# Performance work log

Hardware: AMD Instinct MI355X
Metric: run time of the kernel (lower is better)

The kernel has to match this reference:

```python
import jax, jax.numpy as jnp
import numpy as np

D_MODEL = 256
N_HEAD = 4
HEAD_DIM = D_MODEL // N_HEAD  # 64


def setup_inputs() -> dict:
    key = jax.random.key(0)
    kx, kw, kb = jax.random.split(key, 3)
    x = jax.random.normal(kx, (4, 2048, D_MODEL), dtype=jnp.float32)
    # nn.Linear(256, 768): weight [768, 256], bias [768]
    bound = 1.0 / np.sqrt(D_MODEL)
    W_qkv = jax.random.uniform(kw, (3 * D_MODEL, D_MODEL), dtype=jnp.float32, minval=-bound, maxval=bound)
    b_qkv = jax.random.uniform(kb, (3 * D_MODEL,), dtype=jnp.float32, minval=-bound, maxval=bound)
    return {"x": x, "W_qkv": W_qkv, "b_qkv": b_qkv}


def reference(x, W_qkv, b_qkv):
    B, S, _ = x.shape
    # fused QKV projection: [B, S, 3*D]
    qkv = jnp.einsum("bsd,ed->bse", x, W_qkv) + b_qkv
    q, k, v = jnp.split(qkv, 3, axis=-1)
    # [B, S, D] -> [B, H, S, Dh]
    def to_heads(t):
        return t.reshape(B, S, N_HEAD, HEAD_DIM).transpose(0, 2, 1, 3)
    q, k, v = to_heads(q), to_heads(k), to_heads(v)
    scale = 1.0 / np.sqrt(HEAD_DIM)
    # scores [B, H, S, S]
    scores = jnp.einsum("bhqd,bhkd->bhqk", q, k) * scale
    attn = jax.nn.softmax(scores, axis=-1)
    out = jnp.einsum("bhqk,bhkd->bhqd", attn, v)  # [B, H, S, Dh]
    return out
```

## Files before the change

kernel.cpp:

```cpp
#include <hip/hip_runtime.h>

#define BB 4
#define SS 2048
#define DM 256
#define NH 4
#define DH 64
#define NROW (BB*SS)
#define NE   (3*DM)
#define BH   (BB*NH)
#define HEAD_ELEMS (BH*SS*DH)
#define NQROWS (BH*SS)
#define NKZ 4

typedef _Float16 half_t;
typedef __attribute__((ext_vector_type(8))) _Float16 half8;
typedef __attribute__((ext_vector_type(4))) _Float16 half4;
typedef __attribute__((ext_vector_type(4))) float floatx4;

#define KPAD 72

#define QK_SCALE 0.18033688011112042f
#define EXP2(x) __builtin_amdgcn_exp2f(x)
#define DEFER_THR 8.0f

__global__ __launch_bounds__(256) void prep(const float* __restrict__ x,
                                            const float* __restrict__ W,
                                            half_t* __restrict__ xh,
                                            half_t* __restrict__ xl,
                                            half_t* __restrict__ wh) {
    int gtid = blockIdx.x * 256 + threadIdx.x;
    {
        int i = gtid * 4;
        float4 v = *(const float4*)&x[i];
        half4 h, l;
        h.x = (half_t)v.x; l.x = (half_t)(v.x - (float)h.x);
        h.y = (half_t)v.y; l.y = (half_t)(v.y - (float)h.y);
        h.z = (half_t)v.z; l.z = (half_t)(v.z - (float)h.z);
        h.w = (half_t)v.w; l.w = (half_t)(v.w - (float)h.w);
        *(half4*)&xh[i] = h;
        *(half4*)&xl[i] = l;
    }
    if (gtid < NE * DM / 4) {
        int i = gtid * 4;
        float4 v = *(const float4*)&W[i];
        half4 h;
        h.x = (half_t)v.x; h.y = (half_t)v.y;
        h.z = (half_t)v.z; h.w = (half_t)v.w;
        *(half4*)&wh[i] = h;
    }
}

__global__ __launch_bounds__(256) void qkv_proj(const half_t* __restrict__ xh,
                                                const half_t* __restrict__ xl,
                                                const half_t* __restrict__ whg,
                                                const float* __restrict__ bias,
                                                half_t* __restrict__ qh,
                                                half_t* __restrict__ kh,
                                                half_t* __restrict__ vt) {
    __shared__ __align__(16) half_t Xh[64 * KPAD];
    __shared__ __align__(16) half_t Xl[64 * KPAD];
    __shared__ __align__(16) half_t Wh[64 * KPAD];

    const int rb   = blockIdx.x * 64;
    const int nb   = blockIdx.y * 64;
    const int tid  = threadIdx.x;
    const int wid  = tid >> 6;
    const int lane = tid & 63;
    const int quad = lane >> 4;
    const int col  = lane & 15;

    floatx4 acc[4];
    #pragma unroll
    for (int t = 0; t < 4; ++t) acc[t] = (floatx4){0.f, 0.f, 0.f, 0.f};

    for (int k0 = 0; k0 < DM; k0 += 64) {
        __syncthreads();
        #pragma unroll
        for (int i = 0; i < 2; ++i) {
            int gi = tid + 256 * i;
            int r  = gi >> 3;
            int c8 = (gi & 7) * 8;
            *(half8*)&Xh[r * KPAD + c8] = *(const half8*)&xh[(size_t)(rb + r) * DM + k0 + c8];
            *(half8*)&Xl[r * KPAD + c8] = *(const half8*)&xl[(size_t)(rb + r) * DM + k0 + c8];
            *(half8*)&Wh[r * KPAD + c8] = *(const half8*)&whg[(size_t)(nb + r) * DM + k0 + c8];
        }
        __syncthreads();

        half8 ah0 = *(const half8*)&Xh[(wid * 16 + col) * KPAD + quad * 8];
        half8 ah1 = *(const half8*)&Xh[(wid * 16 + col) * KPAD + 32 + quad * 8];
        half8 al0 = *(const half8*)&Xl[(wid * 16 + col) * KPAD + quad * 8];
        half8 al1 = *(const half8*)&Xl[(wid * 16 + col) * KPAD + 32 + quad * 8];

        #pragma unroll
        for (int t = 0; t < 4; ++t) {
            half8 bh0 = *(const half8*)&Wh[(t * 16 + col) * KPAD + quad * 8];
            half8 bh1 = *(const half8*)&Wh[(t * 16 + col) * KPAD + 32 + quad * 8];
            acc[t] = __builtin_amdgcn_mfma_f32_16x16x32_f16(ah0, bh0, acc[t], 0, 0, 0);
            acc[t] = __builtin_amdgcn_mfma_f32_16x16x32_f16(ah1, bh1, acc[t], 0, 0, 0);
            acc[t] = __builtin_amdgcn_mfma_f32_16x16x32_f16(al0, bh0, acc[t], 0, 0, 0);
            acc[t] = __builtin_amdgcn_mfma_f32_16x16x32_f16(al1, bh1, acc[t], 0, 0, 0);
        }
    }

    const int part = nb >> 8;
    const int mloc = wid * 16 + quad * 4;
    if (part != 2) {
        #pragma unroll
        for (int t = 0; t < 4; ++t) {
            int e    = nb + t * 16 + col;
            float be = bias[e];
            int dm   = e & 255;
            int h    = dm >> 6;
            int dh   = dm & 63;
            #pragma unroll
            for (int r = 0; r < 4; ++r) {
                int row = rb + mloc + r;
                int b   = row >> 11;
                int s   = row & 2047;
                int bh_ = b * NH + h;
                float val = acc[t][r] + be;
                if (part == 0) {
                    qh[((size_t)bh_ * SS + s) * DH + dh] = (half_t)(val * QK_SCALE);
                } else {
                    kh[((size_t)bh_ * SS + s) * DH + dh] = (half_t)val;
                }
            }
        }
    } else {
        __syncthreads();
        #pragma unroll
        for (int t = 0; t < 4; ++t) {
            int e    = nb + t * 16 + col;
            float be = bias[e];
            #pragma unroll
            for (int r = 0; r < 4; ++r)
                Xh[(t * 16 + col) * KPAD + mloc + r] = (half_t)(acc[t][r] + be);
        }
        __syncthreads();
        const int b   = rb >> 11;
        const int s0  = rb & 2047;
        const int h   = (nb >> 6) & 3;
        const int bh_ = b * NH + h;
        #pragma unroll
        for (int i = 0; i < 2; ++i) {
            int idx = tid + 256 * i;
            int rr  = idx >> 3;
            int cc8 = (idx & 7) * 8;
            *(half8*)&vt[((size_t)bh_ * DH + rr) * SS + s0 + cc8] =
                *(const half8*)&Xh[rr * KPAD + cc8];
        }
    }
}

__global__ __launch_bounds__(256) void attn(const half_t* __restrict__ qh,
                                            const half_t* __restrict__ kh,
                                            const half_t* __restrict__ vt,
                                            half_t* __restrict__ pO,
                                            float* __restrict__ mst,
                                            float* __restrict__ lst) {
    __shared__ __align__(16) half_t Ks[64 * KPAD];
    __shared__ __align__(16) half_t Vts[64 * KPAD];

    const int lin  = blockIdx.x + 16 * blockIdx.y + 256 * blockIdx.z;
    const int xcd  = lin & 7;
    const int j    = lin >> 3;
    const int strm = xcd + 8 * (j >> 4);
    const int q0   = (j & 15) * 128;
    const int bh   = strm & 15;
    const int kz   = strm >> 4;

    const size_t base = (size_t)bh * SS * DH;
    const int tid  = threadIdx.x;
    const int wid  = tid >> 6;
    const int lane = tid & 63;
    const int quad = lane >> 4;
    const int col  = lane & 15;
    const int ktBeg = kz * (SS / NKZ);
    const int ktEnd = ktBeg + (SS / NKZ);

    int srr[2], scc[2];
    #pragma unroll
    for (int i = 0; i < 2; ++i) {
        int gi = tid + 256 * i;
        srr[i] = gi >> 3;
        scc[i] = (gi & 7) * 8;
    }

    half8 bq[2][2];
    #pragma unroll
    for (int st = 0; st < 2; ++st) {
        int s = q0 + wid * 32 + st * 16 + col;
        bq[st][0] = *(const half8*)&qh[base + (size_t)s * DH + quad * 8];
        bq[st][1] = *(const half8*)&qh[base + (size_t)s * DH + 32 + quad * 8];
    }

    half8 nk[2], nv[2];
    #pragma unroll
    for (int i = 0; i < 2; ++i) {
        nk[i] = *(const half8*)&kh[base + (size_t)(ktBeg + srr[i]) * DH + scc[i]];
        nv[i] = *(const half8*)&vt[base + (size_t)srr[i] * SS + ktBeg + scc[i]];
    }

    float m_i[2]    = {-3.0e38f, -3.0e38f};
    float l_part[2] = {0.f, 0.f};
    floatx4 o[2][4];
    #pragma unroll
    for (int st = 0; st < 2; ++st)
        #pragma unroll
        for (int dt = 0; dt < 4; ++dt) o[st][dt] = (floatx4){0.f, 0.f, 0.f, 0.f};

    for (int kt = ktBeg; kt < ktEnd; kt += 64) {
        __syncthreads();
        #pragma unroll
        for (int i = 0; i < 2; ++i) {
            *(half8*)&Ks[srr[i] * KPAD + scc[i]]  = nk[i];
            *(half8*)&Vts[srr[i] * KPAD + scc[i]] = nv[i];
        }
        __syncthreads();

        const int ktn = kt + 64;
        if (ktn < ktEnd) {
            #pragma unroll
            for (int i = 0; i < 2; ++i) {
                nk[i] = *(const half8*)&kh[base + (size_t)(ktn + srr[i]) * DH + scc[i]];
                nv[i] = *(const half8*)&vt[base + (size_t)srr[i] * SS + ktn + scc[i]];
            }
        }

        floatx4 sc[2][4];
        #pragma unroll
        for (int t = 0; t < 4; ++t) {
            half8 ak0 = *(const half8*)&Ks[(t * 16 + col) * KPAD + quad * 8];
            half8 ak1 = *(const half8*)&Ks[(t * 16 + col) * KPAD + 32 + quad * 8];
            #pragma unroll
            for (int st = 0; st < 2; ++st) {
                floatx4 c = (floatx4){0.f, 0.f, 0.f, 0.f};
                c = __builtin_amdgcn_mfma_f32_16x16x32_f16(ak0, bq[st][0], c, 0, 0, 0);
                c = __builtin_amdgcn_mfma_f32_16x16x32_f16(ak1, bq[st][1], c, 0, 0, 0);
                sc[st][t] = c;
            }
        }

        half4 pa[2][4];
        #pragma unroll
        for (int st = 0; st < 2; ++st) {
            float mloc = -3.0e38f;
            #pragma unroll
            for (int t = 0; t < 4; ++t) {
                float a = fmaxf(fmaxf(sc[st][t][0], sc[st][t][1]),
                                fmaxf(sc[st][t][2], sc[st][t][3]));
                mloc = fmaxf(mloc, a);
            }
            mloc = fmaxf(mloc, __shfl_xor(mloc, 16));
            mloc = fmaxf(mloc, __shfl_xor(mloc, 32));

            bool skip = __all(mloc <= m_i[st] + DEFER_THR);
            float m_new = skip ? m_i[st] : fmaxf(m_i[st], mloc);

            float rsumL = 0.f;
            #pragma unroll
            for (int t = 0; t < 4; ++t) {
                float p0 = EXP2(sc[st][t][0] - m_new);
                float p1 = EXP2(sc[st][t][1] - m_new);
                float p2 = EXP2(sc[st][t][2] - m_new);
                float p3 = EXP2(sc[st][t][3] - m_new);
                rsumL += p0 + p1 + p2 + p3;
                pa[st][t] = (half4){(half_t)p0, (half_t)p1, (half_t)p2, (half_t)p3};
            }

            if (skip) {
                l_part[st] += rsumL;
            } else {
                float alpha = EXP2(m_i[st] - m_new);
                m_i[st] = m_new;
                l_part[st] = l_part[st] * alpha + rsumL;
                float ar[4];
                #pragma unroll
                for (int i = 0; i < 4; ++i) ar[i] = __shfl(alpha, quad * 4 + i);
                #pragma unroll
                for (int dt = 0; dt < 4; ++dt)
                    #pragma unroll
                    for (int i = 0; i < 4; ++i)
                        o[st][dt][i] *= ar[i];
            }
        }

        #pragma unroll
        for (int t = 0; t < 4; ++t) {
            #pragma unroll
            for (int dt = 0; dt < 4; ++dt) {
                half4 bv = *(const half4*)&Vts[(dt * 16 + col) * KPAD + t * 16 + quad * 4];
                #pragma unroll
                for (int st = 0; st < 2; ++st)
                    o[st][dt] = __builtin_amdgcn_mfma_f32_16x16x16f16(pa[st][t], bv, o[st][dt], 0, 0, 0);
            }
        }
    }

    const size_t pbase = (size_t)kz * HEAD_ELEMS + base;
    #pragma unroll
    for (int st = 0; st < 2; ++st) {
        float l_i = l_part[st] + __shfl_xor(l_part[st], 16);
        l_i += __shfl_xor(l_i, 32);
        float inv = 1.0f / l_i;
        float ir[4];
        #pragma unroll
        for (int i = 0; i < 4; ++i) ir[i] = __shfl(inv, quad * 4 + i);
        #pragma unroll
        for (int dt = 0; dt < 4; ++dt)
            #pragma unroll
            for (int i = 0; i < 4; ++i) {
                int row = q0 + wid * 32 + st * 16 + quad * 4 + i;
                pO[pbase + (size_t)row * DH + dt * 16 + col] = (half_t)(o[st][dt][i] * ir[i]);
            }
        if (quad == 0) {
            int row = q0 + wid * 32 + st * 16 + col;
            int idx = kz * NQROWS + bh * SS + row;
            mst[idx] = m_i[st];
            lst[idx] = l_i;
        }
    }
}

__global__ __launch_bounds__(256) void merge(const half_t* __restrict__ pO,
                                             const float* __restrict__ mst,
                                             const float* __restrict__ lst,
                                             float* __restrict__ out) {
    int gid = blockIdx.x * 256 + threadIdx.x;
    int row = gid >> 3;
    int dc  = (gid & 7) * 8;
    float m[NKZ], l[NKZ];
    #pragma unroll
    for (int p = 0; p < NKZ; ++p) {
        m[p] = mst[p * NQROWS + row];
        l[p] = lst[p * NQROWS + row];
    }
    float M = fmaxf(fmaxf(m[0], m[1]), fmaxf(m[2], m[3]));
    float w[NKZ], wsum = 0.f;
    #pragma unroll
    for (int p = 0; p < NKZ; ++p) { w[p] = l[p] * EXP2(m[p] - M); wsum += w[p]; }
    float inv = 1.0f / wsum;

    float r[8] = {0.f,0.f,0.f,0.f,0.f,0.f,0.f,0.f};
    #pragma unroll
    for (int p = 0; p < NKZ; ++p) {
        float a = w[p] * inv;
        half8 ov = *(const half8*)&pO[(size_t)p * HEAD_ELEMS + (size_t)row * DH + dc];
        #pragma unroll
        for (int e = 0; e < 8; ++e) r[e] += a * (float)ov[e];
    }
    float4 r0 = {r[0], r[1], r[2], r[3]};
    float4 r1 = {r[4], r[5], r[6], r[7]};
    *(float4*)&out[(size_t)row * DH + dc]     = r0;
    *(float4*)&out[(size_t)row * DH + dc + 4] = r1;
}

extern "C" void kernel_launch(void* const* d_in, const int* in_sizes, int n_in,
                              void* d_out, int out_size, void* d_ws, size_t ws_size,
                              hipStream_t stream) {
    const float* x  = (const float*)d_in[0];
    const float* Wq = (const float*)d_in[1];
    const float* bq = (const float*)d_in[2];
    float* out = (float*)d_out;

    half_t* qh  = (half_t*)d_ws;
    half_t* kh  = qh + (size_t)HEAD_ELEMS;
    half_t* vt  = kh + (size_t)HEAD_ELEMS;
    half_t* xh  = vt + (size_t)HEAD_ELEMS;
    half_t* xl  = xh + (size_t)HEAD_ELEMS;
    half_t* whp = xl + (size_t)HEAD_ELEMS;
    half_t* pO  = (half_t*)d_ws + (size_t)6 * HEAD_ELEMS;
    float*  mst = (float*)((char*)d_ws + (size_t)10 * HEAD_ELEMS * 2);
    float*  lst = mst + (size_t)NKZ * NQROWS;

    prep<<<2048, 256, 0, stream>>>(x, Wq, xh, xl, whp);
    qkv_proj<<<dim3(NROW / 64, NE / 64), 256, 0, stream>>>(xh, xl, whp, bq, qh, kh, vt);
    attn<<<dim3(SS / 128, BH, NKZ), 256, 0, stream>>>(qh, kh, vt, pO, mst, lst);
    merge<<<1024, 256, 0, stream>>>(pO, mst, lst, out);
}
```

Baseline: 113.7 us.

## Fuse x fp16 hi/lo split into QKV projection and reuse X tile across output tiles

The fp32 x is now split into fp16 high and low parts inside the projection kernel, which loads a full 64x256 X tile into shared memory once. Each block then loops over three 64-wide output tiles, so the X tile is reused three times. W tiles are prefetched into registers one step ahead. This removes the xh/xl round trip through global memory and shrinks prep to W conversion only, at the cost of more shared memory per block (about 76KB) and a smaller grid of 512 blocks.

```diff
diff --git a/kernel.cpp b/kernel.cpp
--- a/kernel.cpp
+++ b/kernel.cpp
@@ -18,136 +18,158 @@
 typedef __attribute__((ext_vector_type(4))) float floatx4;
 
 #define KPAD 72
+#define XS   264
 
 #define QK_SCALE 0.18033688011112042f
 #define EXP2(x) __builtin_amdgcn_exp2f(x)
 #define DEFER_THR 8.0f
 
-__global__ __launch_bounds__(256) void prep(const float* __restrict__ x,
-                                            const float* __restrict__ W,
-                                            half_t* __restrict__ xh,
-                                            half_t* __restrict__ xl,
+__global__ __launch_bounds__(256) void prep(const float* __restrict__ W,
                                             half_t* __restrict__ wh) {
     int gtid = blockIdx.x * 256 + threadIdx.x;
-    {
-        int i = gtid * 4;
-        float4 v = *(const float4*)&x[i];
+    int i = gtid * 4;
+    float4 v = *(const float4*)&W[i];
+    half4 h;
+    h.x = (half_t)v.x; h.y = (half_t)v.y;
+    h.z = (half_t)v.z; h.w = (half_t)v.w;
+    *(half4*)&wh[i] = h;
+}
+
+__global__ __launch_bounds__(256) void qkv_proj(const float* __restrict__ x,
+                                                const half_t* __restrict__ whg,
+                                                const float* __restrict__ bias,
+                                                half_t* __restrict__ qh,
+                                                half_t* __restrict__ kh,
+                                                half_t* __restrict__ vt) {
+    __shared__ __align__(16) half_t Xh[64 * XS];
+    __shared__ __align__(16) half_t Xl[64 * XS];
+    __shared__ __align__(16) half_t Wh[64 * KPAD];
+
+    const int rb   = blockIdx.x * 64;
+    const int nq   = blockIdx.y;
+    const int tid  = threadIdx.x;
+    const int wid  = tid >> 6;
+    const int lane = tid & 63;
+    const int quad = lane >> 4;
+    const int col  = lane & 15;
+
+    int wr[2], wc[2];
+    #pragma unroll
+    for (int i = 0; i < 2; ++i) {
+        int gi = tid + 256 * i;
+        wr[i] = gi >> 3;
+        wc[i] = (gi & 7) * 8;
+    }
+
+    half8 nw[2];
+    #pragma unroll
+    for (int i = 0; i < 2; ++i)
+        nw[i] = *(const half8*)&whg[(size_t)(nq * 192 + wr[i]) * DM + wc[i]];
+
+    #pragma unroll
+    for (int it = 0; it < 16; ++it) {
+        int gi = tid + 256 * it;
+        int r  = gi >> 6;
+        int c4 = (gi & 63) * 4;
+        float4 v = *(const float4*)&x[(size_t)(rb + r) * DM + c4];
         half4 h, l;
         h.x = (half_t)v.x; l.x = (half_t)(v.x - (float)h.x);
         h.y = (half_t)v.y; l.y = (half_t)(v.y - (float)h.y);
         h.z = (half_t)v.z; l.z = (half_t)(v.z - (float)h.z);
         h.w = (half_t)v.w; l.w = (half_t)(v.w - (float)h.w);
-        *(half4*)&xh[i] = h;
-        *(half4*)&xl[i] = l;
-    }
-    if (gtid < NE * DM / 4) {
-        int i = gtid * 4;
-        float4 v = *(const float4*)&W[i];
-        half4 h;
-        h.x = (half_t)v.x; h.y = (half_t)v.y;
-        h.z = (half_t)v.z; h.w = (half_t)v.w;
-        *(half4*)&wh[i] = h;
-    }
-}
-
-__global__ __launch_bounds__(256) void qkv_proj(const half_t* __restrict__ xh,
-                                                const half_t* __restrict__ xl,
-                                                const half_t* __restrict__ whg,
-                                                const float* __restrict__ bias,
-                                                half_t* __restrict__ qh,
-                                                half_t* __restrict__ kh,
-                                                half_t* __restrict__ vt) {
-    __shared__ __align__(16) half_t Xh[64 * KPAD];
-    __shared__ __align__(16) half_t Xl[64 * KPAD];
-    __shared__ __align__(16) half_t Wh[64 * KPAD];
-
-    const int rb   = blockIdx.x * 64;
-    const int nb   = blockIdx.y * 64;
-    const int tid  = threadIdx.x;
-    const int wid  = tid >> 6;
-    const int lane = tid & 63;
-    const int quad = lane >> 4;
-    const int col  = lane & 15;
-
-    floatx4 acc[4];
-    #pragma unroll
-    for (int t = 0; t < 4; ++t) acc[t] = (floatx4){0.f, 0.f, 0.f, 0.f};
-
-    for (int k0 = 0; k0 < DM; k0 += 64) {
-        __syncthreads();
-        #pragma unroll
-        for (int i = 0; i < 2; ++i) {
-            int gi = tid + 256 * i;
-            int r  = gi >> 3;
-            int c8 = (gi & 7) * 8;
-            *(half8*)&Xh[r * KPAD + c8] = *(const half8*)&xh[(size_t)(rb + r) * DM + k0 + c8];
-            *(half8*)&Xl[r * KPAD + c8] = *(const half8*)&xl[(size_t)(rb + r) * DM + k0 + c8];
-            *(half8*)&Wh[r * KPAD + c8] = *(const half8*)&whg[(size_t)(nb + r) * DM + k0 + c8];
-        }
-        __syncthreads();
-
-        half8 ah0 = *(const half8*)&Xh[(wid * 16 + col) * KPAD + quad * 8];
-        half8 ah1 = *(const half8*)&Xh[(wid * 16 + col) * KPAD + 32 + quad * 8];
-        half8 al0 = *(const half8*)&Xl[(wid * 16 + col) * KPAD + quad * 8];
-        half8 al1 = *(const half8*)&Xl[(wid * 16 + col) * KPAD + 32 + quad * 8];
-
-        #pragma unroll
-        for (int t = 0; t < 4; ++t) {
-            half8 bh0 = *(const half8*)&Wh[(t * 16 + col) * KPAD + quad * 8];
-            half8 bh1 = *(const half8*)&Wh[(t * 16 + col) * KPAD + 32 + quad * 8];
-            acc[t] = __builtin_amdgcn_mfma_f32_16x16x32_f16(ah0, bh0, acc[t], 0, 0, 0);
-            acc[t] = __builtin_amdgcn_mfma_f32_16x16x32_f16(ah1, bh1, acc[t], 0, 0, 0);
-            acc[t] = __builtin_amdgcn_mfma_f32_16x16x32_f16(al0, bh0, acc[t], 0, 0, 0);
-            acc[t] = __builtin_amdgcn_mfma_f32_16x16x32_f16(al1, bh1, acc[t], 0, 0, 0);
-        }
-    }
-
-    const int part = nb >> 8;
-    const int mloc = wid * 16 + quad * 4;
-    if (part != 2) {
-        #pragma unroll
-        for (int t = 0; t < 4; ++t) {
-            int e    = nb + t * 16 + col;
-            float be = bias[e];
-            int dm   = e & 255;
-            int h    = dm >> 6;
-            int dh   = dm & 63;
-            #pragma unroll
-            for (int r = 0; r < 4; ++r) {
-                int row = rb + mloc + r;
-                int b   = row >> 11;
-                int s   = row & 2047;
-                int bh_ = b * NH + h;
-                float val = acc[t][r] + be;
-                if (part == 0) {
-                    qh[((size_t)bh_ * SS + s) * DH + dh] = (half_t)(val * QK_SCALE);
-                } else {
-                    kh[((size_t)bh_ * SS + s) * DH + dh] = (half_t)val;
+        *(half4*)&Xh[r * XS + c4] = h;
+        *(half4*)&Xl[r * XS + c4] = l;
+    }
+    __syncthreads();
+
+    for (int ti = 0; ti < 3; ++ti) {
+        const int nt   = nq * 3 + ti;
+        const int nb   = nt * 64;
+        const int part = nt >> 2;
+
+        floatx4 acc[4];
+        #pragma unroll
+        for (int t = 0; t < 4; ++t) acc[t] = (floatx4){0.f, 0.f, 0.f, 0.f};
+
+        for (int k0i = 0; k0i < 4; ++k0i) {
+            const int k0 = k0i * 64;
+            #pragma unroll
+            for (int i = 0; i < 2; ++i)
+                *(half8*)&Wh[wr[i] * KPAD + wc[i]] = nw[i];
+            __syncthreads();
+
+            int s = ti * 4 + k0i + 1;
+            if (s < 12) {
+                int nrow = nq * 192 + (s >> 2) * 64;
+                int nk0  = (s & 3) * 64;
+                #pragma unroll
+                for (int i = 0; i < 2; ++i)
+                    nw[i] = *(const half8*)&whg[(size_t)(nrow + wr[i]) * DM + nk0 + wc[i]];
+            }
+
+            half8 ah0 = *(const half8*)&Xh[(wid * 16 + col) * XS + k0 + quad * 8];
+            half8 ah1 = *(const half8*)&Xh[(wid * 16 + col) * XS + k0 + 32 + quad * 8];
+            half8 al0 = *(const half8*)&Xl[(wid * 16 + col) * XS + k0 + quad * 8];
+            half8 al1 = *(const half8*)&Xl[(wid * 16 + col) * XS + k0 + 32 + quad * 8];
+
+            #pragma unroll
+            for (int t = 0; t < 4; ++t) {
+                half8 bh0 = *(const half8*)&Wh[(t * 16 + col) * KPAD + quad * 8];
+                half8 bh1 = *(const half8*)&Wh[(t * 16 + col) * KPAD + 32 + quad * 8];
+                acc[t] = __builtin_amdgcn_mfma_f32_16x16x32_f16(ah0, bh0, acc[t], 0, 0, 0);
+                acc[t] = __builtin_amdgcn_mfma_f32_16x16x32_f16(ah1, bh1, acc[t], 0, 0, 0);
+                acc[t] = __builtin_amdgcn_mfma_f32_16x16x32_f16(al0, bh0, acc[t], 0, 0, 0);
+                acc[t] = __builtin_amdgcn_mfma_f32_16x16x32_f16(al1, bh1, acc[t], 0, 0, 0);
+            }
+            __syncthreads();
+        }
+
+        const int mloc = wid * 16 + quad * 4;
+        if (part != 2) {
+            #pragma unroll
+            for (int t = 0; t < 4; ++t) {
+                int e    = nb + t * 16 + col;
+                float be = bias[e];
+                int dm   = e & 255;
+                int h    = dm >> 6;
+                int dh   = dm & 63;
+                #pragma unroll
+                for (int r = 0; r < 4; ++r) {
+                    int row = rb + mloc + r;
+                    int b   = row >> 11;
+                    int s   = row & 2047;
+                    int bh_ = b * NH + h;
+                    float val = acc[t][r] + be;
+                    if (part == 0) {
+                        qh[((size_t)bh_ * SS + s) * DH + dh] = (half_t)(val * QK_SCALE);
+                    } else {
+                        kh[((size_t)bh_ * SS + s) * DH + dh] = (half_t)val;
+                    }
                 }
             }
-        }
-    } else {
-        __syncthreads();
-        #pragma unroll
-        for (int t = 0; t < 4; ++t) {
-            int e    = nb + t * 16 + col;
-            float be = bias[e];
-            #pragma unroll
-            for (int r = 0; r < 4; ++r)
-                Xh[(t * 16 + col) * KPAD + mloc + r] = (half_t)(acc[t][r] + be);
-        }
-        __syncthreads();
-        const int b   = rb >> 11;
-        const int s0  = rb & 2047;
-        const int h   = (nb >> 6) & 3;
-        const int bh_ = b * NH + h;
-        #pragma unroll
-        for (int i = 0; i < 2; ++i) {
-            int idx = tid + 256 * i;
-            int rr  = idx >> 3;
-            int cc8 = (idx & 7) * 8;
-            *(half8*)&vt[((size_t)bh_ * DH + rr) * SS + s0 + cc8] =
-                *(const half8*)&Xh[rr * KPAD + cc8];
+        } else {
+            #pragma unroll
+            for (int t = 0; t < 4; ++t) {
+                int e    = nb + t * 16 + col;
+                float be = bias[e];
+                #pragma unroll
+                for (int r = 0; r < 4; ++r)
+                    Wh[(t * 16 + col) * KPAD + mloc + r] = (half_t)(acc[t][r] + be);
+            }
+            __syncthreads();
+            const int b   = rb >> 11;
+            const int s0  = rb & 2047;
+            const int h   = (nb >> 6) & 3;
+            const int bh_ = b * NH + h;
+            #pragma unroll
+            for (int i = 0; i < 2; ++i) {
+                int idx = tid + 256 * i;
+                int rr  = idx >> 3;
+                int cc8 = (idx & 7) * 8;
+                *(half8*)&vt[((size_t)bh_ * DH + rr) * SS + s0 + cc8] =
+                    *(const half8*)&Wh[rr * KPAD + cc8];
+            }
+            __syncthreads();
         }
     }
 }
@@ -366,15 +388,13 @@
     half_t* qh  = (half_t*)d_ws;
     half_t* kh  = qh + (size_t)HEAD_ELEMS;
     half_t* vt  = kh + (size_t)HEAD_ELEMS;
-    half_t* xh  = vt + (size_t)HEAD_ELEMS;
-    half_t* xl  = xh + (size_t)HEAD_ELEMS;
-    half_t* whp = xl + (size_t)HEAD_ELEMS;
+    half_t* whp = (half_t*)d_ws + (size_t)5 * HEAD_ELEMS;
     half_t* pO  = (half_t*)d_ws + (size_t)6 * HEAD_ELEMS;
     float*  mst = (float*)((char*)d_ws + (size_t)10 * HEAD_ELEMS * 2);
     float*  lst = mst + (size_t)NKZ * NQROWS;
 
-    prep<<<2048, 256, 0, stream>>>(x, Wq, xh, xl, whp);
-    qkv_proj<<<dim3(NROW / 64, NE / 64), 256, 0, stream>>>(xh, xl, whp, bq, qh, kh, vt);
+    prep<<<192, 256, 0, stream>>>(Wq, whp);
+    qkv_proj<<<dim3(128, 4), 256, 0, stream>>>(x, whp, bq, qh, kh, vt);
     attn<<<dim3(SS / 128, BH, NKZ), 256, 0, stream>>>(qh, kh, vt, pO, mst, lst);
     merge<<<1024, 256, 0, stream>>>(pO, mst, lst, out);
 }
```

Measured after the change: 116.4 us. 1.02x slower.
